# Kernel tuning notes

Hardware: AMD Instinct MI355X
Metric: run time of the kernel (lower is better)

Reference implementation:

```python
import jax, jax.numpy as jnp
import numpy as np

B, T, D = 4, 2048, 1024
H = 16
HD = D // H

def setup_inputs() -> dict:
    key = jax.random.key(0)
    k1, k2, k3, k4, k5 = jax.random.split(key, 5)
    x = jax.random.normal(k1, (B, T, D), dtype=jnp.float32)
    scale = 1.0 / np.sqrt(D)
    W_qkv = jax.random.normal(k2, (D, 3 * D), dtype=jnp.float32) * scale
    b_qkv = jnp.zeros((3 * D,), dtype=jnp.float32)
    W_proj = jax.random.normal(k3, (D, D), dtype=jnp.float32) * scale
    b_proj = jnp.zeros((D,), dtype=jnp.float32)
    return {"x": x, "W_qkv": W_qkv, "b_qkv": b_qkv, "W_proj": W_proj, "b_proj": b_proj}

def reference(x, W_qkv, b_qkv, W_proj, b_proj):
    Bx, Tx, C = x.shape
    qkv = x @ W_qkv + b_qkv                      # [B,T,3C]
    q, k, v = jnp.split(qkv, 3, axis=-1)
    # [B,T,H,hd] -> [B,H,T,hd]
    q = q.reshape(Bx, Tx, H, HD).transpose(0, 2, 1, 3)
    k = k.reshape(Bx, Tx, H, HD).transpose(0, 2, 1, 3)
    v = v.reshape(Bx, Tx, H, HD).transpose(0, 2, 1, 3)
    att = jnp.einsum('bhqd,bhkd->bhqk', q, k) / jnp.sqrt(jnp.float32(HD))
    causal = jnp.tril(jnp.ones((Tx, Tx), dtype=bool))
    att = jnp.where(causal[None, None], att, -jnp.inf)
    att = jax.nn.softmax(att, axis=-1)
    y = jnp.einsum('bhqk,bhkd->bhqd', att, v)    # [B,H,T,hd]
    y = y.transpose(0, 2, 1, 3).reshape(Bx, Tx, C)
    return y @ W_proj + b_proj
```

## Files before the change

kernel.cpp:

```cpp
#include <hip/hip_runtime.h>
#include <hip/hip_bf16.h>

#define B_  4
#define T_  2048
#define D_  1024
#define H_  16
#define HD_ 64

typedef short s16x8 __attribute__((ext_vector_type(8)));
typedef short s16x4 __attribute__((ext_vector_type(4)));
typedef float f32x4 __attribute__((ext_vector_type(4)));
typedef unsigned int u32x2 __attribute__((ext_vector_type(2)));

#define MFMA32(a, b, c) __builtin_amdgcn_mfma_f32_16x16x32_bf16(a, b, c, 0, 0, 0)
#define MFMA16(a, b, c) __builtin_amdgcn_mfma_f32_16x16x16bf16_1k(a, b, c, 0, 0, 0)

__device__ __forceinline__ unsigned short f2bf(float f) {
  unsigned u = __builtin_bit_cast(unsigned, f);
  u += 0x7fffu + ((u >> 16) & 1u);
  return (unsigned short)(u >> 16);
}

__device__ __forceinline__ float bf2f(unsigned short h) {
  return __builtin_bit_cast(float, (unsigned)h << 16);
}

#define GLOAD_LDS16(src, dst)                                            \
  __builtin_amdgcn_global_load_lds(                                      \
      (__attribute__((address_space(1))) void*)(void*)(src),             \
      (__attribute__((address_space(3))) void*)(dst), 16, 0, 0)

__global__ __launch_bounds__(256) void convert_x_kernel(
    const float* __restrict__ in, unsigned short* __restrict__ out, int n8) {
  int i = blockIdx.x * 256 + threadIdx.x;
  if (i >= n8) return;
  const float4* p = ((const float4*)in) + (size_t)i * 2;
  float4 a = p[0], b = p[1];
  s16x8 o;
  o[0] = (short)f2bf(a.x); o[1] = (short)f2bf(a.y);
  o[2] = (short)f2bf(a.z); o[3] = (short)f2bf(a.w);
  o[4] = (short)f2bf(b.x); o[5] = (short)f2bf(b.y);
  o[6] = (short)f2bf(b.z); o[7] = (short)f2bf(b.w);
  *(((s16x8*)out) + i) = o;
}

__global__ __launch_bounds__(256) void transpose_w_kernel(
    const float* __restrict__ W, unsigned short* __restrict__ Wt, int K, int N) {
  __shared__ float tile[32][33];
  int n0 = blockIdx.x * 32, k0 = blockIdx.y * 32;
  int tx = threadIdx.x & 31, ty = threadIdx.x >> 5;
#pragma unroll
  for (int j = 0; j < 4; ++j) {
    int k = ty + j * 8;
    tile[k][tx] = W[(size_t)(k0 + k) * N + n0 + tx];
  }
  __syncthreads();
#pragma unroll
  for (int j = 0; j < 4; ++j) {
    int n = ty + j * 8;
    Wt[(size_t)(n0 + n) * K + k0 + tx] = f2bf(tile[tx][n]);
  }
}

template <int OUTF32>
__global__ __launch_bounds__(256) void gemm_kernel(
    const unsigned short* __restrict__ A, const unsigned short* __restrict__ Bt,
    const float* __restrict__ bias, void* __restrict__ Cout, int M, int N, int K) {
  __shared__ char lds[32768];
  char* Al = lds;
  char* Bl = lds + 16384;
  const int n0 = blockIdx.x * 128, m0 = blockIdx.y * 128;
  const int w = threadIdx.x >> 6, lane = threadIdx.x & 63;
  const int l15 = lane & 15, g = lane >> 4;
  const int wr = w >> 1, wc = w & 1;
  const int srow = (lane >> 3);
  const int u = lane & 7;
  const int soct = (u ^ srow) << 3;
  const int rx = l15 & 7;
  f32x4 acc[4][4] = {};

  for (int kt = 0; kt < K; kt += 64) {
    __syncthreads();
#pragma unroll
    for (int i = 0; i < 4; ++i) {
      int c = w * 4 + i;
      int row = c * 8 + srow;
      const unsigned short* srcA = A + (size_t)(m0 + row) * K + kt + soct;
      GLOAD_LDS16(srcA, Al + c * 1024);
      const unsigned short* srcB = Bt + (size_t)(n0 + row) * K + kt + soct;
      GLOAD_LDS16(srcB, Bl + c * 1024);
    }
    __syncthreads();
#pragma unroll
    for (int kk = 0; kk < 2; ++kk) {
      const int roct = ((kk * 4 + g) ^ rx) << 4;
      s16x8 af[4], bfr[4];
#pragma unroll
      for (int mi = 0; mi < 4; ++mi) {
        int row = wr * 64 + mi * 16 + l15;
        af[mi] = *(const s16x8*)(Al + row * 128 + roct);
      }
#pragma unroll
      for (int ni = 0; ni < 4; ++ni) {
        int row = wc * 64 + ni * 16 + l15;
        bfr[ni] = *(const s16x8*)(Bl + row * 128 + roct);
      }
#pragma unroll
      for (int mi = 0; mi < 4; ++mi)
#pragma unroll
        for (int ni = 0; ni < 4; ++ni)
          acc[mi][ni] = MFMA32(af[mi], bfr[ni], acc[mi][ni]);
    }
  }
#pragma unroll
  for (int ni = 0; ni < 4; ++ni) {
    int col = n0 + wc * 64 + ni * 16 + l15;
    float bv = bias[col];
#pragma unroll
    for (int mi = 0; mi < 4; ++mi) {
      int row = m0 + wr * 64 + mi * 16 + g * 4;
#pragma unroll
      for (int r = 0; r < 4; ++r) {
        float v = acc[mi][ni][r] + bv;
        if (OUTF32)
          ((float*)Cout)[(size_t)(row + r) * N + col] = v;
        else
          ((unsigned short*)Cout)[(size_t)(row + r) * N + col] = f2bf(v);
      }
    }
  }
}

#define VT_STR 76
#define VT_BLK 1232
__global__ __launch_bounds__(256, 4) void attn_kernel(
    const unsigned short* __restrict__ qkv, unsigned short* __restrict__ yatt) {
  __shared__ char lds[8192 + 4 * VT_BLK * 2];
  const int bx = blockIdx.x;
  const int bh = blockIdx.y;
  const int b = bh >> 4, h = bh & 15;
  const int w = threadIdx.x >> 6;
  const int lane = threadIdx.x & 63;
  const int l15 = lane & 15, g = lane >> 4;

  const size_t rowstride = 3 * D_;
  const unsigned short* Qb = qkv + (size_t)b * T_ * rowstride + h * HD_;
  const unsigned short* Kb = Qb + D_;
  const unsigned short* Vb = Qb + 2 * D_;

  char* Klds = lds;
  unsigned short* Vt = (unsigned short*)(lds + 8192);

  const int krow0 = (w * 2 + 0) * 8 + (lane >> 3);
  const int krow1 = (w * 2 + 1) * 8 + (lane >> 3);
  const int u = lane & 7;
  const int vkey = w * 16 + (lane >> 2);
  const int vdb = lane & 3;
  const float SC = 0.18033688011112042f;
  const s16x4 onesf = {(short)0x3F80, (short)0x3F80, (short)0x3F80, (short)0x3F80};

  const int qtA = 31 - bx;
  const int nA = qtA + 1;

  s16x8 kc0, kc1, vc0, vc1;
  s16x8 kn0, kn1, vn0, vn1;

  auto ld = [&](int kt, s16x8& a, s16x8& b2, s16x8& c, s16x8& d2) {
    const unsigned short* kb = Kb + (size_t)(kt * 64) * rowstride;
    a = *(const s16x8*)(kb + (size_t)krow0 * rowstride + u * 8);
    b2 = *(const s16x8*)(kb + (size_t)krow1 * rowstride + u * 8);
    const unsigned short* vs = Vb + (size_t)(kt * 64 + vkey) * rowstride + vdb * 16;
    c = *(const s16x8*)(vs);
    d2 = *(const s16x8*)(vs + 8);
  };

  ld(0, kc0, kc1, vc0, vc1);
  ld(1, kn0, kn1, vn0, vn1);
  int f = 0;

#pragma unroll 1
  for (int ti = 0; ti < 2; ++ti) {
    const int qt = ti ? bx : qtA;
    s16x8 qf0, qf1;
    {
      const unsigned short* qr = Qb + (size_t)(qt * 64 + w * 16 + l15) * rowstride;
      s16x8 a0 = *(const s16x8*)(qr + g * 8);
      s16x8 a1 = *(const s16x8*)(qr + 32 + g * 8);
#pragma unroll
      for (int j = 0; j < 8; ++j) {
        qf0[j] = (short)f2bf(bf2f((unsigned short)a0[j]) * SC);
        qf1[j] = (short)f2bf(bf2f((unsigned short)a1[j]) * SC);
      }
    }
    float m = -1e30f;
    f32x4 acc[4] = {};
    f32x4 accS = {};

#pragma unroll 1
    for (int kt = 0; kt <= qt; ++kt) {
      __syncthreads();
      *(s16x8*)(Klds + krow0 * 128 + ((u ^ (krow0 & 7)) << 4)) = kc0;
      *(s16x8*)(Klds + krow1 * 128 + ((u ^ (krow1 & 7)) << 4)) = kc1;
#pragma unroll
      for (int j = 0; j < 8; ++j) {
        Vt[vdb * VT_BLK + j * VT_STR + vkey] = (unsigned short)vc0[j];
        Vt[vdb * VT_BLK + (8 + j) * VT_STR + vkey] = (unsigned short)vc1[j];
      }
      __syncthreads();
      kc0 = kn0; kc1 = kn1; vc0 = vn0; vc1 = vn1;
      {
        int f2 = f + 2;
        if (f2 < 33) {
          int kt2 = (f2 < nA) ? f2 : f2 - nA;
          ld(kt2, kn0, kn1, vn0, vn1);
        }
      }

      float tv[16];
      __builtin_amdgcn_s_setprio(1);
#pragma unroll
      for (int kk = 0; kk < 4; ++kk) {
        int key = kk * 16 + l15;
        const s16x8 kf0 = *(const s16x8*)(Klds + key * 128 + ((g ^ (key & 7)) << 4));
        const s16x8 kf1 = *(const s16x8*)(Klds + key * 128 + (((4 + g) ^ (key & 7)) << 4));
        f32x4 s = {};
        s = MFMA32(kf0, qf0, s);
        s = MFMA32(kf1, qf1, s);
#pragma unroll
        for (int r = 0; r < 4; ++r) tv[kk * 4 + r] = s[r];
      }
      __builtin_amdgcn_s_setprio(0);
      if (kt == qt) {
        int q = qt * 64 + w * 16 + l15;
#pragma unroll
        for (int kk = 0; kk < 4; ++kk)
#pragma unroll
          for (int r = 0; r < 4; ++r)
            if (kt * 64 + kk * 16 + g * 4 + r > q) tv[kk * 4 + r] = -1e30f;
      }
      float a0 = fmaxf(fmaxf(tv[0], tv[1]), tv[2]);
      float a1 = fmaxf(fmaxf(tv[3], tv[4]), tv[5]);
      float a2 = fmaxf(fmaxf(tv[6], tv[7]), tv[8]);
      float a3 = fmaxf(fmaxf(tv[9], tv[10]), tv[11]);
      float a4 = fmaxf(fmaxf(tv[12], tv[13]), tv[14]);
      float b0 = fmaxf(fmaxf(a0, a1), a2);
      float b1 = fmaxf(fmaxf(a3, a4), tv[15]);
      float tm = fmaxf(b0, b1);
      tm = fmaxf(tm, __shfl_xor(tm, 16));
      tm = fmaxf(tm, __shfl_xor(tm, 32));
      if (!__all(tm - m <= 8.0f)) {
        float mn = fmaxf(m, tm);
        float corr = exp2f(m - mn);
        m = mn;
#pragma unroll
        for (int i = 0; i < 4; ++i) {
          acc[i][0] *= corr; acc[i][1] *= corr;
          acc[i][2] *= corr; acc[i][3] *= corr;
        }
        accS[0] *= corr; accS[1] *= corr; accS[2] *= corr; accS[3] *= corr;
      }
      s16x4 pb[4];
#pragma unroll
      for (int kk = 0; kk < 4; ++kk) {
        float p0 = exp2f(tv[kk * 4 + 0] - m), p1 = exp2f(tv[kk * 4 + 1] - m);
        float p2 = exp2f(tv[kk * 4 + 2] - m), p3 = exp2f(tv[kk * 4 + 3] - m);
        u32x2 pk;
        pk[0] = __builtin_amdgcn_perm(__builtin_bit_cast(unsigned, p1),
                                      __builtin_bit_cast(unsigned, p0), 0x07060302u);
        pk[1] = __builtin_amdgcn_perm(__builtin_bit_cast(unsigned, p3),
                                      __builtin_bit_cast(unsigned, p2), 0x07060302u);
        pb[kk] = __builtin_bit_cast(s16x4, pk);
      }
      __builtin_amdgcn_s_setprio(1);
#pragma unroll
      for (int kk = 0; kk < 4; ++kk) {
#pragma unroll
        for (int db = 0; db < 4; ++db) {
          s16x4 vf = *(const s16x4*)(Vt + db * VT_BLK + l15 * VT_STR + kk * 16 + g * 4);
          acc[db] = MFMA16(vf, pb[kk], acc[db]);
        }
        accS = MFMA16(onesf, pb[kk], accS);
      }
      __builtin_amdgcn_s_setprio(0);
      ++f;
    }

    float inv = 1.0f / accS[0];
    __syncthreads();
    unsigned short* ylds = (unsigned short*)lds;
#pragma unroll
    for (int db = 0; db < 4; ++db)
#pragma unroll
      for (int r = 0; r < 4; ++r)
        ylds[(db * 16 + g * 4 + r) * 66 + w * 16 + l15] = f2bf(acc[db][r] * inv);
    __syncthreads();
    int qq = threadIdx.x >> 2;
    int dc = (threadIdx.x & 3) * 16;
    s16x8 o1, o2;
#pragma unroll
    for (int j = 0; j < 8; ++j) {
      o1[j] = (short)ylds[(dc + j) * 66 + qq];
      o2[j] = (short)ylds[(dc + 8 + j) * 66 + qq];
    }
    unsigned short* dst = yatt + (size_t)(b * T_ + qt * 64 + qq) * D_ + h * HD_ + dc;
    *(s16x8*)(dst) = o1;
    *(s16x8*)(dst + 8) = o2;
  }
}

extern "C" void kernel_launch(void* const* d_in, const int* in_sizes, int n_in,
                              void* d_out, int out_size, void* d_ws, size_t ws_size,
                              hipStream_t stream) {
  const float* x     = (const float*)d_in[0];
  const float* Wqkv  = (const float*)d_in[1];
  const float* bqkv  = (const float*)d_in[2];
  const float* Wproj = (const float*)d_in[3];
  const float* bproj = (const float*)d_in[4];
  float* out = (float*)d_out;

  unsigned short* xb   = (unsigned short*)d_ws;
  unsigned short* Wqb  = xb + (size_t)8192 * 1024;
  unsigned short* Wpb  = Wqb + (size_t)3072 * 1024;
  unsigned short* qkvb = Wpb + (size_t)1024 * 1024;
  unsigned short* yb   = xb;

  convert_x_kernel<<<dim3(4096), dim3(256), 0, stream>>>(x, xb, 8192 * 1024 / 8);
  transpose_w_kernel<<<dim3(96, 32), dim3(256), 0, stream>>>(Wqkv, Wqb, 1024, 3072);
  transpose_w_kernel<<<dim3(32, 32), dim3(256), 0, stream>>>(Wproj, Wpb, 1024, 1024);
  gemm_kernel<0><<<dim3(24, 64), dim3(256), 0, stream>>>(xb, Wqb, bqkv, qkvb, 8192, 3072, 1024);
  attn_kernel<<<dim3(16, 64), dim3(256), 0, stream>>>(qkvb, yb);
  gemm_kernel<1><<<dim3(8, 64), dim3(256), 0, stream>>>(yb, Wpb, bproj, out, 8192, 1024, 1024);
}
```

Baseline: 194.2 us.

## Enlarge attention query tile to 128 rows, two 16-row groups per wave

The attention kernel now processes 128 query rows per tile instead of 64, with each wave holding two 16-row Q fragments that share every K and V tile loaded into LDS. The grid shrinks to 8x64 blocks, the causal pairing still balances a long and a short tile per block, and key tiles past a wave's rows are skipped after the shared staging step. This halves K/V global loads and LDS staging per query but doubles the accumulator registers, so launch bounds drop to 2 blocks per CU and fewer blocks are launched.

```diff
diff --git a/kernel.cpp b/kernel.cpp
--- a/kernel.cpp
+++ b/kernel.cpp
@@ -133,9 +133,9 @@
 
 #define VT_STR 76
 #define VT_BLK 1232
-__global__ __launch_bounds__(256, 4) void attn_kernel(
+__global__ __launch_bounds__(256, 2) void attn_kernel(
     const unsigned short* __restrict__ qkv, unsigned short* __restrict__ yatt) {
-  __shared__ char lds[8192 + 4 * VT_BLK * 2];
+  __shared__ char lds[18048];
   const int bx = blockIdx.x;
   const int bh = blockIdx.y;
   const int b = bh >> 4, h = bh & 15;
@@ -159,8 +159,8 @@
   const float SC = 0.18033688011112042f;
   const s16x4 onesf = {(short)0x3F80, (short)0x3F80, (short)0x3F80, (short)0x3F80};
 
-  const int qtA = 31 - bx;
-  const int nA = qtA + 1;
+  const int qtA_t = 15 - bx;
+  const int nA = 2 * qtA_t + 2;
 
   s16x8 kc0, kc1, vc0, vc1;
   s16x8 kn0, kn1, vn0, vn1;
@@ -180,24 +180,31 @@
 
 #pragma unroll 1
   for (int ti = 0; ti < 2; ++ti) {
-    const int qt = ti ? bx : qtA;
-    s16x8 qf0, qf1;
+    const int qt = ti ? bx : qtA_t;
+    const int ntk = 2 * qt + 2;
+    const int base = qt * 128 + w * 32;
+    s16x8 qfA0, qfA1, qfB0, qfB1;
     {
-      const unsigned short* qr = Qb + (size_t)(qt * 64 + w * 16 + l15) * rowstride;
-      s16x8 a0 = *(const s16x8*)(qr + g * 8);
-      s16x8 a1 = *(const s16x8*)(qr + 32 + g * 8);
+      const unsigned short* qa = Qb + (size_t)(base + l15) * rowstride;
+      const unsigned short* qb = Qb + (size_t)(base + 16 + l15) * rowstride;
+      s16x8 a0 = *(const s16x8*)(qa + g * 8);
+      s16x8 a1 = *(const s16x8*)(qa + 32 + g * 8);
+      s16x8 b0 = *(const s16x8*)(qb + g * 8);
+      s16x8 b1 = *(const s16x8*)(qb + 32 + g * 8);
 #pragma unroll
       for (int j = 0; j < 8; ++j) {
-        qf0[j] = (short)f2bf(bf2f((unsigned short)a0[j]) * SC);
-        qf1[j] = (short)f2bf(bf2f((unsigned short)a1[j]) * SC);
-      }
-    }
-    float m = -1e30f;
-    f32x4 acc[4] = {};
-    f32x4 accS = {};
+        qfA0[j] = (short)f2bf(bf2f((unsigned short)a0[j]) * SC);
+        qfA1[j] = (short)f2bf(bf2f((unsigned short)a1[j]) * SC);
+        qfB0[j] = (short)f2bf(bf2f((unsigned short)b0[j]) * SC);
+        qfB1[j] = (short)f2bf(bf2f((unsigned short)b1[j]) * SC);
+      }
+    }
+    float mA = -1e30f, mB = -1e30f;
+    f32x4 accA[4] = {}, accB[4] = {};
+    f32x4 accSA = {}, accSB = {};
 
 #pragma unroll 1
-    for (int kt = 0; kt <= qt; ++kt) {
+    for (int kt = 0; kt < ntk; ++kt) {
       __syncthreads();
       *(s16x8*)(Klds + krow0 * 128 + ((u ^ (krow0 & 7)) << 4)) = kc0;
       *(s16x8*)(Klds + krow1 * 128 + ((u ^ (krow1 & 7)) << 4)) = kc1;
@@ -210,66 +217,106 @@
       kc0 = kn0; kc1 = kn1; vc0 = vn0; vc1 = vn1;
       {
         int f2 = f + 2;
-        if (f2 < 33) {
+        if (f2 < 34) {
           int kt2 = (f2 < nA) ? f2 : f2 - nA;
           ld(kt2, kn0, kn1, vn0, vn1);
         }
       }
-
-      float tv[16];
+      ++f;
+
+      if (kt * 64 > base + 31) continue;
+
+      float tvA[16], tvB[16];
       __builtin_amdgcn_s_setprio(1);
 #pragma unroll
       for (int kk = 0; kk < 4; ++kk) {
         int key = kk * 16 + l15;
         const s16x8 kf0 = *(const s16x8*)(Klds + key * 128 + ((g ^ (key & 7)) << 4));
         const s16x8 kf1 = *(const s16x8*)(Klds + key * 128 + (((4 + g) ^ (key & 7)) << 4));
-        f32x4 s = {};
-        s = MFMA32(kf0, qf0, s);
-        s = MFMA32(kf1, qf1, s);
-#pragma unroll
-        for (int r = 0; r < 4; ++r) tv[kk * 4 + r] = s[r];
+        f32x4 sA = {}, sB = {};
+        sA = MFMA32(kf0, qfA0, sA);
+        sA = MFMA32(kf1, qfA1, sA);
+        sB = MFMA32(kf0, qfB0, sB);
+        sB = MFMA32(kf1, qfB1, sB);
+#pragma unroll
+        for (int r = 0; r < 4; ++r) { tvA[kk * 4 + r] = sA[r]; tvB[kk * 4 + r] = sB[r]; }
       }
       __builtin_amdgcn_s_setprio(0);
-      if (kt == qt) {
-        int q = qt * 64 + w * 16 + l15;
+      if (kt * 64 + 63 > base) {
+        int qA = base + l15, qB = base + 16 + l15;
 #pragma unroll
         for (int kk = 0; kk < 4; ++kk)
 #pragma unroll
-          for (int r = 0; r < 4; ++r)
-            if (kt * 64 + kk * 16 + g * 4 + r > q) tv[kk * 4 + r] = -1e30f;
-      }
-      float a0 = fmaxf(fmaxf(tv[0], tv[1]), tv[2]);
-      float a1 = fmaxf(fmaxf(tv[3], tv[4]), tv[5]);
-      float a2 = fmaxf(fmaxf(tv[6], tv[7]), tv[8]);
-      float a3 = fmaxf(fmaxf(tv[9], tv[10]), tv[11]);
-      float a4 = fmaxf(fmaxf(tv[12], tv[13]), tv[14]);
-      float b0 = fmaxf(fmaxf(a0, a1), a2);
-      float b1 = fmaxf(fmaxf(a3, a4), tv[15]);
-      float tm = fmaxf(b0, b1);
-      tm = fmaxf(tm, __shfl_xor(tm, 16));
-      tm = fmaxf(tm, __shfl_xor(tm, 32));
-      if (!__all(tm - m <= 8.0f)) {
-        float mn = fmaxf(m, tm);
-        float corr = exp2f(m - mn);
-        m = mn;
-#pragma unroll
-        for (int i = 0; i < 4; ++i) {
-          acc[i][0] *= corr; acc[i][1] *= corr;
-          acc[i][2] *= corr; acc[i][3] *= corr;
-        }
-        accS[0] *= corr; accS[1] *= corr; accS[2] *= corr; accS[3] *= corr;
-      }
-      s16x4 pb[4];
-#pragma unroll
-      for (int kk = 0; kk < 4; ++kk) {
-        float p0 = exp2f(tv[kk * 4 + 0] - m), p1 = exp2f(tv[kk * 4 + 1] - m);
-        float p2 = exp2f(tv[kk * 4 + 2] - m), p3 = exp2f(tv[kk * 4 + 3] - m);
-        u32x2 pk;
-        pk[0] = __builtin_amdgcn_perm(__builtin_bit_cast(unsigned, p1),
-                                      __builtin_bit_cast(unsigned, p0), 0x07060302u);
-        pk[1] = __builtin_amdgcn_perm(__builtin_bit_cast(unsigned, p3),
-                                      __builtin_bit_cast(unsigned, p2), 0x07060302u);
-        pb[kk] = __builtin_bit_cast(s16x4, pk);
+          for (int r = 0; r < 4; ++r) {
+            int key = kt * 64 + kk * 16 + g * 4 + r;
+            if (key > qA) tvA[kk * 4 + r] = -1e30f;
+            if (key > qB) tvB[kk * 4 + r] = -1e30f;
+          }
+      }
+      s16x4 pbA[4], pbB[4];
+      {
+        float a0 = fmaxf(fmaxf(tvA[0], tvA[1]), tvA[2]);
+        float a1 = fmaxf(fmaxf(tvA[3], tvA[4]), tvA[5]);
+        float a2 = fmaxf(fmaxf(tvA[6], tvA[7]), tvA[8]);
+        float a3 = fmaxf(fmaxf(tvA[9], tvA[10]), tvA[11]);
+        float a4 = fmaxf(fmaxf(tvA[12], tvA[13]), tvA[14]);
+        float tm = fmaxf(fmaxf(fmaxf(a0, a1), a2), fmaxf(fmaxf(a3, a4), tvA[15]));
+        tm = fmaxf(tm, __shfl_xor(tm, 16));
+        tm = fmaxf(tm, __shfl_xor(tm, 32));
+        if (!__all(tm - mA <= 8.0f)) {
+          float mn = fmaxf(mA, tm);
+          float corr = exp2f(mA - mn);
+          mA = mn;
+#pragma unroll
+          for (int i = 0; i < 4; ++i) {
+            accA[i][0] *= corr; accA[i][1] *= corr;
+            accA[i][2] *= corr; accA[i][3] *= corr;
+          }
+          accSA[0] *= corr; accSA[1] *= corr; accSA[2] *= corr; accSA[3] *= corr;
+        }
+#pragma unroll
+        for (int kk = 0; kk < 4; ++kk) {
+          float p0 = exp2f(tvA[kk * 4 + 0] - mA), p1 = exp2f(tvA[kk * 4 + 1] - mA);
+          float p2 = exp2f(tvA[kk * 4 + 2] - mA), p3 = exp2f(tvA[kk * 4 + 3] - mA);
+          u32x2 pk;
+          pk[0] = __builtin_amdgcn_perm(__builtin_bit_cast(unsigned, p1),
+                                        __builtin_bit_cast(unsigned, p0), 0x07060302u);
+          pk[1] = __builtin_amdgcn_perm(__builtin_bit_cast(unsigned, p3),
+                                        __builtin_bit_cast(unsigned, p2), 0x07060302u);
+          pbA[kk] = __builtin_bit_cast(s16x4, pk);
+        }
+      }
+      {
+        float a0 = fmaxf(fmaxf(tvB[0], tvB[1]), tvB[2]);
+        float a1 = fmaxf(fmaxf(tvB[3], tvB[4]), tvB[5]);
+        float a2 = fmaxf(fmaxf(tvB[6], tvB[7]), tvB[8]);
+        float a3 = fmaxf(fmaxf(tvB[9], tvB[10]), tvB[11]);
+        float a4 = fmaxf(fmaxf(tvB[12], tvB[13]), tvB[14]);
+        float tm = fmaxf(fmaxf(fmaxf(a0, a1), a2), fmaxf(fmaxf(a3, a4), tvB[15]));
+        tm = fmaxf(tm, __shfl_xor(tm, 16));
+        tm = fmaxf(tm, __shfl_xor(tm, 32));
+        if (!__all(tm - mB <= 8.0f)) {
+          float mn = fmaxf(mB, tm);
+          float corr = exp2f(mB - mn);
+          mB = mn;
+#pragma unroll
+          for (int i = 0; i < 4; ++i) {
+            accB[i][0] *= corr; accB[i][1] *= corr;
+            accB[i][2] *= corr; accB[i][3] *= corr;
+          }
+          accSB[0] *= corr; accSB[1] *= corr; accSB[2] *= corr; accSB[3] *= corr;
+        }
+#pragma unroll
+        for (int kk = 0; kk < 4; ++kk) {
+          float p0 = exp2f(tvB[kk * 4 + 0] - mB), p1 = exp2f(tvB[kk * 4 + 1] - mB);
+          float p2 = exp2f(tvB[kk * 4 + 2] - mB), p3 = exp2f(tvB[kk * 4 + 3] - mB);
+          u32x2 pk;
+          pk[0] = __builtin_amdgcn_perm(__builtin_bit_cast(unsigned, p1),
+                                        __builtin_bit_cast(unsigned, p0), 0x07060302u);
+          pk[1] = __builtin_amdgcn_perm(__builtin_bit_cast(unsigned, p3),
+                                        __builtin_bit_cast(unsigned, p2), 0x07060302u);
+          pbB[kk] = __builtin_bit_cast(s16x4, pk);
+        }
       }
       __builtin_amdgcn_s_setprio(1);
 #pragma unroll
@@ -277,34 +324,46 @@
 #pragma unroll
         for (int db = 0; db < 4; ++db) {
           s16x4 vf = *(const s16x4*)(Vt + db * VT_BLK + l15 * VT_STR + kk * 16 + g * 4);
-          acc[db] = MFMA16(vf, pb[kk], acc[db]);
-        }
-        accS = MFMA16(onesf, pb[kk], accS);
+          accA[db] = MFMA16(vf, pbA[kk], accA[db]);
+          accB[db] = MFMA16(vf, pbB[kk], accB[db]);
+        }
+        accSA = MFMA16(onesf, pbA[kk], accSA);
+        accSB = MFMA16(onesf, pbB[kk], accSB);
       }
       __builtin_amdgcn_s_setprio(0);
-      ++f;
-    }
-
-    float inv = 1.0f / accS[0];
+    }
+
+    float invA = 1.0f / accSA[0];
+    float invB = 1.0f / accSB[0];
     __syncthreads();
     unsigned short* ylds = (unsigned short*)lds;
 #pragma unroll
     for (int db = 0; db < 4; ++db)
 #pragma unroll
-      for (int r = 0; r < 4; ++r)
-        ylds[(db * 16 + g * 4 + r) * 66 + w * 16 + l15] = f2bf(acc[db][r] * inv);
+      for (int r = 0; r < 4; ++r) {
+        int d = db * 16 + g * 4 + r;
+        ylds[d * 130 + w * 32 + l15] = f2bf(accA[db][r] * invA);
+        ylds[d * 130 + w * 32 + 16 + l15] = f2bf(accB[db][r] * invB);
+      }
     __syncthreads();
-    int qq = threadIdx.x >> 2;
-    int dc = (threadIdx.x & 3) * 16;
-    s16x8 o1, o2;
-#pragma unroll
-    for (int j = 0; j < 8; ++j) {
-      o1[j] = (short)ylds[(dc + j) * 66 + qq];
-      o2[j] = (short)ylds[(dc + 8 + j) * 66 + qq];
-    }
-    unsigned short* dst = yatt + (size_t)(b * T_ + qt * 64 + qq) * D_ + h * HD_ + dc;
-    *(s16x8*)(dst) = o1;
-    *(s16x8*)(dst + 8) = o2;
+    {
+      int qq = threadIdx.x >> 1;
+      int dc = (threadIdx.x & 1) * 32;
+      s16x8 o0, o1, o2, o3;
+#pragma unroll
+      for (int j = 0; j < 8; ++j) {
+        o0[j] = (short)ylds[(dc + j) * 130 + qq];
+        o1[j] = (short)ylds[(dc + 8 + j) * 130 + qq];
+        o2[j] = (short)ylds[(dc + 16 + j) * 130 + qq];
+        o3[j] = (short)ylds[(dc + 24 + j) * 130 + qq];
+      }
+      unsigned short* dst =
+          yatt + (size_t)(b * T_ + qt * 128 + qq) * D_ + h * HD_ + dc;
+      *(s16x8*)(dst) = o0;
+      *(s16x8*)(dst + 8) = o1;
+      *(s16x8*)(dst + 16) = o2;
+      *(s16x8*)(dst + 24) = o3;
+    }
   }
 }
 
@@ -328,6 +387,6 @@
   transpose_w_kernel<<<dim3(96, 32), dim3(256), 0, stream>>>(Wqkv, Wqb, 1024, 3072);
   transpose_w_kernel<<<dim3(32, 32), dim3(256), 0, stream>>>(Wproj, Wpb, 1024, 1024);
   gemm_kernel<0><<<dim3(24, 64), dim3(256), 0, stream>>>(xb, Wqb, bqkv, qkvb, 8192, 3072, 1024);
-  attn_kernel<<<dim3(16, 64), dim3(256), 0, stream>>>(qkvb, yb);
+  attn_kernel<<<dim3(8, 64), dim3(256), 0, stream>>>(qkvb, yb);
   gemm_kernel<1><<<dim3(8, 64), dim3(256), 0, stream>>>(yb, Wpb, bproj, out, 8192, 1024, 1024);
 }
```

Result: no change. 193.2 us (-0.5%).
